# Kernel optimization log

Measured on AMD Instinct MI355X. Metric: run time of the kernel, lower is better.

Reference implementation:

```python
import jax, jax.numpy as jnp
import numpy as np

D = 768
N_HEAD = 12
HEAD_D = D // N_HEAD


def setup_inputs() -> dict:
    key = jax.random.key(0)
    ks = jax.random.split(key, 9)
    s = 1.0 / np.sqrt(D)
    inp = {
        "x": jax.random.normal(ks[0], (2, 2048, D), dtype=jnp.float32),
        "Wq": jax.random.normal(ks[1], (D, D), dtype=jnp.float32) * s,
        "bq": jnp.zeros((D,), dtype=jnp.float32),
        "Wk": jax.random.normal(ks[2], (D, D), dtype=jnp.float32) * s,
        "bk": jnp.zeros((D,), dtype=jnp.float32),
        "Wv": jax.random.normal(ks[3], (D, D), dtype=jnp.float32) * s,
        "bv": jnp.zeros((D,), dtype=jnp.float32),
        "Wo": jax.random.normal(ks[4], (D, D), dtype=jnp.float32) * s,
        "bo": jnp.zeros((D,), dtype=jnp.float32),
    }
    return inp


def reference(x, Wq, bq, Wk, bk, Wv, bv, Wo, bo):
    B, S, _ = x.shape
    # projections; split heads -> [B, H, S, hd]
    def heads(t):
        return t.reshape(B, S, N_HEAD, HEAD_D).transpose(0, 2, 1, 3)
    q = heads(x @ Wq.T + bq)
    k = heads(x @ Wk.T + bk)
    v = heads(x @ Wv.T + bv)
    scale = 1.0 / np.sqrt(HEAD_D)
    scores = jnp.einsum("bhqd,bhkd->bhqk", q, k) * scale  # [B,H,S,S]
    causal = jnp.tril(jnp.ones((S, S), dtype=bool))
    scores = jnp.where(causal, scores, jnp.float32(-jnp.inf))
    attn = jax.nn.softmax(scores, axis=-1)
    out = jnp.einsum("bhqk,bhkd->bhqd", attn, v)
    out = out.transpose(0, 2, 1, 3).reshape(B, S, D)
    return out @ Wo.T + bo
```

## Files before the change

kernel.cpp:

```cpp
#include <hip/hip_runtime.h>
#include <hip/hip_bf16.h>

#define BD 2
#define SLEN 2048
#define DDIM 768
#define HNUM 12
#define HD 64
#define MROWS (BD * SLEN)

using short4v = __attribute__((ext_vector_type(4))) short;
using short8 = __attribute__((ext_vector_type(8))) short;
using f32x4 = __attribute__((ext_vector_type(4))) float;
using uint4v = __attribute__((ext_vector_type(4))) unsigned int;

__device__ __forceinline__ short f2bf(float f) {
  __hip_bfloat16 h = __float2bfloat16(f);
  return *reinterpret_cast<short*>(&h);
}
__device__ __forceinline__ float bf2f(short s) {
  unsigned int u = ((unsigned int)(unsigned short)s) << 16;
  float f;
  __builtin_memcpy(&f, &u, 4);
  return f;
}
__device__ __forceinline__ unsigned pkbf(float a, float b) {
  return (unsigned)(unsigned short)f2bf(a) |
         ((unsigned)(unsigned short)f2bf(b) << 16);
}
__device__ __forceinline__ void gload16(const short* g, short* l) {
  __builtin_amdgcn_global_load_lds(
      (const __attribute__((address_space(1))) unsigned int*)g,
      (__attribute__((address_space(3))) unsigned int*)l, 16, 0, 0);
}

#define P_ELEM ((size_t)MROWS * DDIM)
#define PW_ELEM ((size_t)DDIM * DDIM)

__global__ __launch_bounds__(256) void cvt_split(
    const float* __restrict__ x, const float* __restrict__ Wq,
    const float* __restrict__ Wk, const float* __restrict__ Wv,
    const float* __restrict__ Wo, short* __restrict__ ws) {
  const float* src;
  short* hi;
  size_t n;
  switch (blockIdx.z) {
    case 0:  src = x;  hi = ws;                             n = P_ELEM;  break;
    case 1:  src = Wq; hi = ws + 2 * P_ELEM;                n = PW_ELEM; break;
    case 2:  src = Wk; hi = ws + 2 * P_ELEM + 2 * PW_ELEM;  n = PW_ELEM; break;
    case 3:  src = Wv; hi = ws + 2 * P_ELEM + 4 * PW_ELEM;  n = PW_ELEM; break;
    default: src = Wo; hi = ws + 2 * P_ELEM + 6 * PW_ELEM;  n = PW_ELEM; break;
  }
  short* lo = hi + n;
  const size_t n4 = n >> 2;
  for (size_t i = (size_t)blockIdx.x * 256 + threadIdx.x; i < n4;
       i += (size_t)gridDim.x * 256) {
    float4 f = ((const float4*)src)[i];
    short4v h, l;
    h[0] = f2bf(f.x); h[1] = f2bf(f.y); h[2] = f2bf(f.z); h[3] = f2bf(f.w);
    l[0] = f2bf(f.x - bf2f(h[0]));
    l[1] = f2bf(f.y - bf2f(h[1]));
    l[2] = f2bf(f.z - bf2f(h[2]));
    l[3] = f2bf(f.w - bf2f(h[3]));
    ((short4v*)hi)[i] = h;
    ((short4v*)lo)[i] = l;
  }
}

template <int BM, int BN, int MODE>
__device__ __forceinline__ void gemm3_body(
    const short* __restrict__ Ah, const short* __restrict__ Al,
    const short* __restrict__ Bh, const short* __restrict__ Bl,
    const float* __restrict__ bias, float scale, void* __restrict__ outp) {
  __shared__ short As[2][2][BM][32];
  __shared__ short Bs[2][2][BN][32];

  const int n0 = blockIdx.x * BN;
  const int m0 = blockIdx.y * BM;
  const int t = threadIdx.x;
  const int w = t >> 6, l = t & 63;
  const int wm = w >> 1, wn = w & 1;
  const int x = l & 15, g = l >> 4;

  constexpr int NI = BM / 32, NJ = BN / 32;
  constexpr int QA = BM / 64;
  constexpr int QB = BN / 64;

  f32x4 acc[NI][NJ];
  #pragma unroll
  for (int i = 0; i < NI; ++i)
    #pragma unroll
    for (int j = 0; j < NJ; ++j) acc[i][j] = (f32x4){0.f, 0.f, 0.f, 0.f};

  auto stage = [&](int bb, int k0) {
    #pragma unroll
    for (int q = 0; q < QA; ++q) {
      const int local = q * 256 + t;
      const int row = local >> 2;
      const int ks = (local & 3) ^ ((row >> 1) & 3);
      const int lbase = (q * 256 + (t & 192)) * 8;
      const size_t go = (size_t)(m0 + row) * DDIM + k0 + ks * 8;
      gload16(Ah + go, &As[bb][0][0][0] + lbase);
      gload16(Al + go, &As[bb][1][0][0] + lbase);
    }
    #pragma unroll
    for (int q = 0; q < QB; ++q) {
      const int local = q * 256 + t;
      const int row = local >> 2;
      const int ks = (local & 3) ^ ((row >> 1) & 3);
      const int lbase = (q * 256 + (t & 192)) * 8;
      const size_t go = (size_t)(n0 + row) * DDIM + k0 + ks * 8;
      gload16(Bh + go, &Bs[bb][0][0][0] + lbase);
      gload16(Bl + go, &Bs[bb][1][0][0] + lbase);
    }
  };

  stage(0, 0);
  int cur = 0;
  for (int k0 = 0; k0 < DDIM; k0 += 32) {
    __syncthreads();
    if (k0 + 32 < DDIM) stage(cur ^ 1, k0 + 32);

    short8 af[2][NI], bf[2][NJ];
    #pragma unroll
    for (int i = 0; i < NI; ++i) {
      const int row = wm * (BM / 2) + i * 16 + x;
      const int ks = g ^ ((row >> 1) & 3);
      af[0][i] = *(const short8*)&As[cur][0][row][ks * 8];
      af[1][i] = *(const short8*)&As[cur][1][row][ks * 8];
    }
    #pragma unroll
    for (int j = 0; j < NJ; ++j) {
      const int row = wn * (BN / 2) + j * 16 + x;
      const int ks = g ^ ((row >> 1) & 3);
      bf[0][j] = *(const short8*)&Bs[cur][0][row][ks * 8];
      bf[1][j] = *(const short8*)&Bs[cur][1][row][ks * 8];
    }
    __builtin_amdgcn_s_setprio(1);
    #pragma unroll
    for (int i = 0; i < NI; ++i)
      #pragma unroll
      for (int j = 0; j < NJ; ++j) {
        acc[i][j] = __builtin_amdgcn_mfma_f32_16x16x32_bf16(af[0][i], bf[0][j], acc[i][j], 0, 0, 0);
        acc[i][j] = __builtin_amdgcn_mfma_f32_16x16x32_bf16(af[0][i], bf[1][j], acc[i][j], 0, 0, 0);
        acc[i][j] = __builtin_amdgcn_mfma_f32_16x16x32_bf16(af[1][i], bf[0][j], acc[i][j], 0, 0, 0);
      }
    __builtin_amdgcn_s_setprio(0);
    cur ^= 1;
  }

  #pragma unroll
  for (int j = 0; j < NJ; ++j) {
    const int n = n0 + wn * (BN / 2) + j * 16 + x;
    const float bj = bias[n];
    #pragma unroll
    for (int i = 0; i < NI; ++i) {
      #pragma unroll
      for (int reg = 0; reg < 4; ++reg) {
        const int m = m0 + wm * (BM / 2) + i * 16 + 4 * g + reg;
        const float v = (acc[i][j][reg] + bj) * scale;
        if (MODE == 0) {
          ((float*)outp)[(size_t)m * DDIM + n] = v;
        } else {
          const int b_ = m >> 11, s_ = m & (SLEN - 1);
          const int h_ = n >> 6, d_ = n & (HD - 1);
          ((short*)outp)[(((size_t)(b_ * HNUM + h_) * SLEN + s_) * HD) + d_] = f2bf(v);
        }
      }
    }
  }
}

__global__ __launch_bounds__(256, 2) void gemm_qkv3(
    const short* __restrict__ ws, const float* __restrict__ bq,
    const float* __restrict__ bk, const float* __restrict__ bv,
    short* __restrict__ Qb, short* __restrict__ Kb, short* __restrict__ Vb) {
  const short* Ah = ws;
  const short* Al = ws + P_ELEM;
  const short* Bh;
  const float* bias;
  short* out;
  float scale;
  switch (blockIdx.z) {
    case 0:  Bh = ws + 2 * P_ELEM;                bias = bq; out = Qb; scale = 0.125f; break;
    case 1:  Bh = ws + 2 * P_ELEM + 2 * PW_ELEM;  bias = bk; out = Kb; scale = 1.f;   break;
    default: Bh = ws + 2 * P_ELEM + 4 * PW_ELEM;  bias = bv; out = Vb; scale = 1.f;   break;
  }
  gemm3_body<128, 128, 1>(Ah, Al, Bh, Bh + PW_ELEM, bias, scale, out);
}

__global__ __launch_bounds__(256, 2) void gemm_out3(
    const short* __restrict__ AOh, const short* __restrict__ AOl,
    const short* __restrict__ Wh, const short* __restrict__ Wl,
    const float* __restrict__ bias, float* __restrict__ out) {
  gemm3_body<64, 64, 0>(AOh, AOl, Wh, Wl, bias, 1.f, out);
}

__global__ __launch_bounds__(256) void flash_fwd_mfma(
    const short* __restrict__ Q, const short* __restrict__ K,
    const short* __restrict__ V, short* __restrict__ AOh,
    short* __restrict__ AOl) {
  const int bh = blockIdx.x;
  const int qt = 31 - (int)blockIdx.y;
  const int b = bh / HNUM, h = bh % HNUM;
  const int t = threadIdx.x;
  const int w = t >> 6, l = t & 63;
  const int x = l & 15, g = l >> 4;
  const int q0 = qt * 64;
  const int qrow = q0 + 16 * w + x;

  __shared__ short Klds[128][72];
  __shared__ short Vlds[64][138];

  short8 Qf[2];
  {
    const short* qp = Q + ((size_t)bh * SLEN + qrow) * HD;
    Qf[0] = *(const short8*)(qp + 8 * g);
    Qf[1] = *(const short8*)(qp + 8 * g + 32);
  }

  f32x4 Oacc[4];
  #pragma unroll
  for (int dc = 0; dc < 4; ++dc) Oacc[dc] = (f32x4){0.f, 0.f, 0.f, 0.f};
  float m_run = -1e30f, l_run = 0.f;

  const int ntiles = qt / 2 + 1;

  short8 krg[4], vrg[4];
  auto load_tile = [&](int kt) {
    const size_t rowb = (size_t)bh * SLEN + (size_t)kt * 128;
    #pragma unroll
    for (int q = 0; q < 4; ++q) {
      const int c = q * 256 + t;
      krg[q] = *(const short8*)(K + (rowb + (c >> 3)) * HD + (c & 7) * 8);
      vrg[q] = *(const short8*)(V + (rowb + (c >> 3)) * HD + (c & 7) * 8);
    }
  };

  load_tile(0);
  for (int kt = 0; kt < ntiles; ++kt) {
    __syncthreads();
    #pragma unroll
    for (int q = 0; q < 4; ++q) {
      const int c = q * 256 + t;
      *(short8*)&Klds[c >> 3][(c & 7) * 8] = krg[q];
      const int j = c >> 3, d0 = (c & 7) * 8;
      #pragma unroll
      for (int i = 0; i < 8; ++i) Vlds[d0 + i][j] = vrg[q][i];
    }
    if (kt + 1 < ntiles) load_tile(kt + 1);
    __syncthreads();

    f32x4 S[8];
    __builtin_amdgcn_s_setprio(1);
    #pragma unroll
    for (int jt = 0; jt < 8; ++jt) {
      short8 Kf0 = *(const short8*)&Klds[16 * jt + x][8 * g];
      short8 Kf1 = *(const short8*)&Klds[16 * jt + x][8 * g + 32];
      f32x4 z = (f32x4){0.f, 0.f, 0.f, 0.f};
      z = __builtin_amdgcn_mfma_f32_16x16x32_bf16(Kf0, Qf[0], z, 0, 0, 0);
      S[jt] = __builtin_amdgcn_mfma_f32_16x16x32_bf16(Kf1, Qf[1], z, 0, 0, 0);
    }
    __builtin_amdgcn_s_setprio(0);

    if (kt == ntiles - 1) {
      const int jb = kt * 128 + 4 * g;
      #pragma unroll
      for (int jt = 0; jt < 8; ++jt)
        #pragma unroll
        for (int r = 0; r < 4; ++r)
          if (jb + 16 * jt + r > qrow) S[jt][r] = -1e30f;
    }

    float tm = -1e30f;
    #pragma unroll
    for (int jt = 0; jt < 8; ++jt)
      #pragma unroll
      for (int r = 0; r < 4; ++r) tm = fmaxf(tm, S[jt][r]);
    tm = fmaxf(tm, __shfl_xor(tm, 16));
    tm = fmaxf(tm, __shfl_xor(tm, 32));
    const float mn = fmaxf(m_run, tm);
    const float resc = __expf(m_run - mn);
    m_run = mn;
    float ts = 0.f;
    #pragma unroll
    for (int jt = 0; jt < 8; ++jt)
      #pragma unroll
      for (int r = 0; r < 4; ++r) {
        const float p = __expf(S[jt][r] - mn);
        S[jt][r] = p;
        ts += p;
      }
    ts += __shfl_xor(ts, 16);
    ts += __shfl_xor(ts, 32);
    l_run = l_run * resc + ts;
    #pragma unroll
    for (int dc = 0; dc < 4; ++dc) Oacc[dc] *= resc;

    uint4v PA[4];
    const bool hihalf = (g >= 2);
    const bool oddg = (g & 1);
    #pragma unroll
    for (int c = 0; c < 4; ++c) {
      const unsigned e_lo = pkbf(S[2 * c][0], S[2 * c][1]);
      const unsigned e_hi = pkbf(S[2 * c][2], S[2 * c][3]);
      const unsigned o_lo = pkbf(S[2 * c + 1][0], S[2 * c + 1][1]);
      const unsigned o_hi = pkbf(S[2 * c + 1][2], S[2 * c + 1][3]);
      const unsigned xe_lo = (unsigned)__shfl_xor((int)e_lo, 32);
      const unsigned xe_hi = (unsigned)__shfl_xor((int)e_hi, 32);
      const unsigned xo_lo = (unsigned)__shfl_xor((int)o_lo, 32);
      const unsigned xo_hi = (unsigned)__shfl_xor((int)o_hi, 32);
      const unsigned ap_lo = hihalf ? xo_lo : e_lo;
      const unsigned ap_hi = hihalf ? xo_hi : e_hi;
      const unsigned bp_lo = hihalf ? o_lo : xe_lo;
      const unsigned bp_hi = hihalf ? o_hi : xe_hi;
      const unsigned sa_lo = (unsigned)__shfl_xor((int)ap_lo, 16);
      const unsigned sa_hi = (unsigned)__shfl_xor((int)ap_hi, 16);
      const unsigned sb_lo = (unsigned)__shfl_xor((int)bp_lo, 16);
      const unsigned sb_hi = (unsigned)__shfl_xor((int)bp_hi, 16);
      PA[c][0] = oddg ? sb_lo : ap_lo;
      PA[c][1] = oddg ? sb_hi : ap_hi;
      PA[c][2] = oddg ? bp_lo : sa_lo;
      PA[c][3] = oddg ? bp_hi : sa_hi;
    }

    __builtin_amdgcn_s_setprio(1);
    #pragma unroll
    for (int dc = 0; dc < 4; ++dc) {
      #pragma unroll
      for (int c = 0; c < 4; ++c) {
        short8 Vf = *(const short8*)&Vlds[16 * dc + x][32 * c + 8 * g];
        Oacc[dc] = __builtin_amdgcn_mfma_f32_16x16x32_bf16(
            Vf, *(const short8*)&PA[c], Oacc[dc], 0, 0, 0);
      }
    }
    __builtin_amdgcn_s_setprio(0);
  }

  const float inv = 1.f / l_run;
  const size_t base = ((size_t)(b * SLEN + qrow)) * DDIM + h * HD + 4 * g;
  #pragma unroll
  for (int dc = 0; dc < 4; ++dc) {
    short4v hi4, lo4;
    #pragma unroll
    for (int r = 0; r < 4; ++r) {
      const float v = Oacc[dc][r] * inv;
      const short hh = f2bf(v);
      hi4[r] = hh;
      lo4[r] = f2bf(v - bf2f(hh));
    }
    *(short4v*)(AOh + base + 16 * dc) = hi4;
    *(short4v*)(AOl + base + 16 * dc) = lo4;
  }
}

extern "C" void kernel_launch(void* const* d_in, const int* in_sizes, int n_in,
                              void* d_out, int out_size, void* d_ws, size_t ws_size,
                              hipStream_t stream) {
  const float* x  = (const float*)d_in[0];
  const float* Wq = (const float*)d_in[1];
  const float* bq = (const float*)d_in[2];
  const float* Wk = (const float*)d_in[3];
  const float* bk = (const float*)d_in[4];
  const float* Wv = (const float*)d_in[5];
  const float* bv = (const float*)d_in[6];
  const float* Wo = (const float*)d_in[7];
  const float* bo = (const float*)d_in[8];
  float* out = (float*)d_out;

  short* S = (short*)d_ws;
  short* AOh = S;
  short* AOl = S + P_ELEM;
  const short* Wo_h = S + 2 * P_ELEM + 6 * PW_ELEM;
  const short* Wo_l = Wo_h + PW_ELEM;
  short* Qb = S + 2 * P_ELEM + 8 * PW_ELEM;
  short* Kb = Qb + P_ELEM;
  short* Vb = Kb + P_ELEM;

  dim3 blk(256);
  cvt_split<<<dim3(768, 1, 5), blk, 0, stream>>>(x, Wq, Wk, Wv, Wo, S);
  gemm_qkv3<<<dim3(DDIM / 128, MROWS / 128, 3), blk, 0, stream>>>(
      S, bq, bk, bv, Qb, Kb, Vb);
  flash_fwd_mfma<<<dim3(BD * HNUM, SLEN / 64), blk, 0, stream>>>(
      Qb, Kb, Vb, AOh, AOl);
  gemm_out3<<<dim3(DDIM / 64, MROWS / 64), blk, 0, stream>>>(
      AOh, AOl, Wo_h, Wo_l, bo, out);
}
```

Baseline: 222.4 us.

## Store low-part bf16 operands in MFMA fragment layout and load directly to registers

The low halves of the split-bf16 operands are now written by the conversion and attention kernels in a per-16-row-tile MFMA fragment layout. The GEMMs load them straight from global memory into registers instead of staging them through LDS. This halves the LDS footprint and traffic, which lets the GEMMs raise occupancy to 3 blocks per SM and switch the QKV tile to 128x96. It adds uncached global fragment loads inside the k-loop and a scattered store layout in the producer kernels.

```diff
diff --git a/kernel.cpp b/kernel.cpp
--- a/kernel.cpp
+++ b/kernel.cpp
@@ -7,6 +7,7 @@
 #define HNUM 12
 #define HD 64
 #define MROWS (BD * SLEN)
+#define KC_N (DDIM / 32)
 
 using short4v = __attribute__((ext_vector_type(4))) short;
 using short8 = __attribute__((ext_vector_type(8))) short;
@@ -31,6 +32,10 @@
   __builtin_amdgcn_global_load_lds(
       (const __attribute__((address_space(1))) unsigned int*)g,
       (__attribute__((address_space(3))) unsigned int*)l, 16, 0, 0);
+}
+
+__device__ __forceinline__ size_t frag_off(int tile, int kc, int lane8) {
+  return ((size_t)tile * KC_N + kc) * 512 + lane8;
 }
 
 #define P_ELEM ((size_t)MROWS * DDIM)
@@ -62,17 +67,22 @@
     l[2] = f2bf(f.z - bf2f(h[2]));
     l[3] = f2bf(f.w - bf2f(h[3]));
     ((short4v*)hi)[i] = h;
-    ((short4v*)lo)[i] = l;
+    const int f0 = (int)(i << 2);
+    const int row = f0 / DDIM, k = f0 % DDIM;
+    const size_t lof = frag_off(row >> 4, k >> 5,
+                                ((((k >> 3) & 3) << 4) + (row & 15)) * 8) +
+                       (k & 7);
+    *(short4v*)(lo + lof) = l;
   }
 }
 
 template <int BM, int BN, int MODE>
 __device__ __forceinline__ void gemm3_body(
-    const short* __restrict__ Ah, const short* __restrict__ Al,
-    const short* __restrict__ Bh, const short* __restrict__ Bl,
+    const short* __restrict__ Ah, const short* __restrict__ Alo,
+    const short* __restrict__ Bh, const short* __restrict__ Blo,
     const float* __restrict__ bias, float scale, void* __restrict__ outp) {
-  __shared__ short As[2][2][BM][32];
-  __shared__ short Bs[2][2][BN][32];
+  __shared__ short As[2][BM][32];
+  __shared__ short Bs[2][BN][32];
 
   const int n0 = blockIdx.x * BN;
   const int m0 = blockIdx.y * BM;
@@ -81,68 +91,80 @@
   const int wm = w >> 1, wn = w & 1;
   const int x = l & 15, g = l >> 4;
 
-  constexpr int NI = BM / 32, NJ = BN / 32;
-  constexpr int QA = BM / 64;
-  constexpr int QB = BN / 64;
-
-  f32x4 acc[NI][NJ];
+  constexpr int NI = BM / 64;
+  constexpr int NJ = BN / 32;
+  constexpr int ACH = BM * 4;
+  constexpr int BCH = BN * 4;
+
+  f32x4 acc[NI * 2][NJ];
   #pragma unroll
-  for (int i = 0; i < NI; ++i)
+  for (int i = 0; i < NI * 2; ++i)
     #pragma unroll
     for (int j = 0; j < NJ; ++j) acc[i][j] = (f32x4){0.f, 0.f, 0.f, 0.f};
 
   auto stage = [&](int bb, int k0) {
     #pragma unroll
-    for (int q = 0; q < QA; ++q) {
-      const int local = q * 256 + t;
-      const int row = local >> 2;
-      const int ks = (local & 3) ^ ((row >> 1) & 3);
-      const int lbase = (q * 256 + (t & 192)) * 8;
-      const size_t go = (size_t)(m0 + row) * DDIM + k0 + ks * 8;
-      gload16(Ah + go, &As[bb][0][0][0] + lbase);
-      gload16(Al + go, &As[bb][1][0][0] + lbase);
-    }
-    #pragma unroll
-    for (int q = 0; q < QB; ++q) {
-      const int local = q * 256 + t;
-      const int row = local >> 2;
-      const int ks = (local & 3) ^ ((row >> 1) & 3);
-      const int lbase = (q * 256 + (t & 192)) * 8;
-      const size_t go = (size_t)(n0 + row) * DDIM + k0 + ks * 8;
-      gload16(Bh + go, &Bs[bb][0][0][0] + lbase);
-      gload16(Bl + go, &Bs[bb][1][0][0] + lbase);
+    for (int q = 0; q < (ACH + 255) / 256; ++q) {
+      const int c = q * 256 + t;
+      if (ACH % 256 == 0 || c < ACH) {
+        const int row = c >> 2;
+        const int ks = (c & 3) ^ ((row >> 1) & 3);
+        gload16(Ah + (size_t)(m0 + row) * DDIM + k0 + ks * 8,
+                &As[bb][0][0] + (q * 256 + (t & 192)) * 8);
+      }
+    }
+    #pragma unroll
+    for (int q = 0; q < (BCH + 255) / 256; ++q) {
+      const int c = q * 256 + t;
+      if (BCH % 256 == 0 || c < BCH) {
+        const int row = c >> 2;
+        const int ks = (c & 3) ^ ((row >> 1) & 3);
+        gload16(Bh + (size_t)(n0 + row) * DDIM + k0 + ks * 8,
+                &Bs[bb][0][0] + (q * 256 + (t & 192)) * 8);
+      }
     }
   };
 
+  const int l8 = l * 8;
   stage(0, 0);
   int cur = 0;
   for (int k0 = 0; k0 < DDIM; k0 += 32) {
+    const int kc = k0 >> 5;
+    short8 alo[NI * 2], blo[NJ];
+    #pragma unroll
+    for (int i = 0; i < NI * 2; ++i) {
+      const int mt = (m0 >> 4) + wm * (BM / 32) + i;
+      alo[i] = *(const short8*)(Alo + frag_off(mt, kc, l8));
+    }
+    #pragma unroll
+    for (int j = 0; j < NJ; ++j) {
+      const int nt = (n0 >> 4) + wn * (BN / 32) + j;
+      blo[j] = *(const short8*)(Blo + frag_off(nt, kc, l8));
+    }
     __syncthreads();
     if (k0 + 32 < DDIM) stage(cur ^ 1, k0 + 32);
 
-    short8 af[2][NI], bf[2][NJ];
-    #pragma unroll
-    for (int i = 0; i < NI; ++i) {
+    short8 afh[NI * 2], bfh[NJ];
+    #pragma unroll
+    for (int i = 0; i < NI * 2; ++i) {
       const int row = wm * (BM / 2) + i * 16 + x;
       const int ks = g ^ ((row >> 1) & 3);
-      af[0][i] = *(const short8*)&As[cur][0][row][ks * 8];
-      af[1][i] = *(const short8*)&As[cur][1][row][ks * 8];
+      afh[i] = *(const short8*)&As[cur][row][ks * 8];
     }
     #pragma unroll
     for (int j = 0; j < NJ; ++j) {
       const int row = wn * (BN / 2) + j * 16 + x;
       const int ks = g ^ ((row >> 1) & 3);
-      bf[0][j] = *(const short8*)&Bs[cur][0][row][ks * 8];
-      bf[1][j] = *(const short8*)&Bs[cur][1][row][ks * 8];
+      bfh[j] = *(const short8*)&Bs[cur][row][ks * 8];
     }
     __builtin_amdgcn_s_setprio(1);
     #pragma unroll
-    for (int i = 0; i < NI; ++i)
+    for (int i = 0; i < NI * 2; ++i)
       #pragma unroll
       for (int j = 0; j < NJ; ++j) {
-        acc[i][j] = __builtin_amdgcn_mfma_f32_16x16x32_bf16(af[0][i], bf[0][j], acc[i][j], 0, 0, 0);
-        acc[i][j] = __builtin_amdgcn_mfma_f32_16x16x32_bf16(af[0][i], bf[1][j], acc[i][j], 0, 0, 0);
-        acc[i][j] = __builtin_amdgcn_mfma_f32_16x16x32_bf16(af[1][i], bf[0][j], acc[i][j], 0, 0, 0);
+        acc[i][j] = __builtin_amdgcn_mfma_f32_16x16x32_bf16(afh[i], bfh[j], acc[i][j], 0, 0, 0);
+        acc[i][j] = __builtin_amdgcn_mfma_f32_16x16x32_bf16(afh[i], blo[j], acc[i][j], 0, 0, 0);
+        acc[i][j] = __builtin_amdgcn_mfma_f32_16x16x32_bf16(alo[i], bfh[j], acc[i][j], 0, 0, 0);
       }
     __builtin_amdgcn_s_setprio(0);
     cur ^= 1;
@@ -153,7 +175,7 @@
     const int n = n0 + wn * (BN / 2) + j * 16 + x;
     const float bj = bias[n];
     #pragma unroll
-    for (int i = 0; i < NI; ++i) {
+    for (int i = 0; i < NI * 2; ++i) {
       #pragma unroll
       for (int reg = 0; reg < 4; ++reg) {
         const int m = m0 + wm * (BM / 2) + i * 16 + 4 * g + reg;
@@ -170,12 +192,12 @@
   }
 }
 
-__global__ __launch_bounds__(256, 2) void gemm_qkv3(
+__global__ __launch_bounds__(256, 3) void gemm_qkv3(
     const short* __restrict__ ws, const float* __restrict__ bq,
     const float* __restrict__ bk, const float* __restrict__ bv,
     short* __restrict__ Qb, short* __restrict__ Kb, short* __restrict__ Vb) {
   const short* Ah = ws;
-  const short* Al = ws + P_ELEM;
+  const short* Alo = ws + P_ELEM;
   const short* Bh;
   const float* bias;
   short* out;
@@ -185,10 +207,10 @@
     case 1:  Bh = ws + 2 * P_ELEM + 2 * PW_ELEM;  bias = bk; out = Kb; scale = 1.f;   break;
     default: Bh = ws + 2 * P_ELEM + 4 * PW_ELEM;  bias = bv; out = Vb; scale = 1.f;   break;
   }
-  gemm3_body<128, 128, 1>(Ah, Al, Bh, Bh + PW_ELEM, bias, scale, out);
-}
-
-__global__ __launch_bounds__(256, 2) void gemm_out3(
+  gemm3_body<128, 96, 1>(Ah, Alo, Bh, Bh + PW_ELEM, bias, scale, out);
+}
+
+__global__ __launch_bounds__(256, 3) void gemm_out3(
     const short* __restrict__ AOh, const short* __restrict__ AOl,
     const short* __restrict__ Wh, const short* __restrict__ Wl,
     const float* __restrict__ bias, float* __restrict__ out) {
@@ -337,7 +359,8 @@
   }
 
   const float inv = 1.f / l_run;
-  const size_t base = ((size_t)(b * SLEN + qrow)) * DDIM + h * HD + 4 * g;
+  const size_t baseh = ((size_t)(b * SLEN + qrow)) * DDIM + h * HD + 4 * g;
+  const int mt = b * 128 + 4 * qt + w;
   #pragma unroll
   for (int dc = 0; dc < 4; ++dc) {
     short4v hi4, lo4;
@@ -348,8 +371,12 @@
       hi4[r] = hh;
       lo4[r] = f2bf(v - bf2f(hh));
     }
-    *(short4v*)(AOh + base + 16 * dc) = hi4;
-    *(short4v*)(AOl + base + 16 * dc) = lo4;
+    *(short4v*)(AOh + baseh + 16 * dc) = hi4;
+    const size_t lof =
+        frag_off(mt, 2 * h + (dc >> 1),
+                 ((2 * (dc & 1) + (g >> 1)) * 16 + x) * 8) +
+        4 * (g & 1);
+    *(short4v*)(AOl + lof) = lo4;
   }
 }
 
@@ -378,7 +405,7 @@
 
   dim3 blk(256);
   cvt_split<<<dim3(768, 1, 5), blk, 0, stream>>>(x, Wq, Wk, Wv, Wo, S);
-  gemm_qkv3<<<dim3(DDIM / 128, MROWS / 128, 3), blk, 0, stream>>>(
+  gemm_qkv3<<<dim3(DDIM / 96, MROWS / 128, 3), blk, 0, stream>>>(
       S, bq, bk, bv, Qb, Kb, Vb);
   flash_fwd_mfma<<<dim3(BD * HNUM, SLEN / 64), blk, 0, stream>>>(
       Qb, Kb, Vb, AOh, AOl);
```

Result: faster. 205.7 us (-7.5%).
